# Performance work log

Measured on AMD Instinct MI355X. Metric: run time of the kernel, lower is better.

## Reference

```python
import jax, jax.numpy as jnp
import numpy as np

B, C, H, W = 32, 512, 32, 32  # in_dims = token_dim = 512, num_heads = 1
D = 512  # token_dim * num_heads
EPS = 1e-12  # torch F.normalize eps


def l2norm(x, axis):
    n = jnp.sqrt(jnp.sum(x * x, axis=axis, keepdims=True))
    return x / jnp.maximum(n, EPS)


def setup_inputs() -> dict:
    key = jax.random.key(0)
    ks = jax.random.split(key, 10)
    s = 1.0 / np.sqrt(D)
    return {
        "x_4d": jax.random.normal(ks[0], (B, C, H, W), dtype=jnp.float32),
        "Wq": jax.random.uniform(ks[1], (D, D), jnp.float32, -s, s),
        "bq": jax.random.uniform(ks[2], (D,), jnp.float32, -s, s),
        "Wk": jax.random.uniform(ks[3], (D, D), jnp.float32, -s, s),
        "bk": jax.random.uniform(ks[4], (D,), jnp.float32, -s, s),
        "w_g": jax.random.normal(ks[5], (D, 1), dtype=jnp.float32),
        "Wp": jax.random.uniform(ks[6], (D, D), jnp.float32, -s, s),
        "bp": jax.random.uniform(ks[7], (D,), jnp.float32, -s, s),
        "Wf": jax.random.uniform(ks[8], (D, D), jnp.float32, -s, s),
        "bf": jax.random.uniform(ks[9], (D,), jnp.float32, -s, s),
    }


def reference(x_4d, Wq, bq, Wk, bk, w_g, Wp, bp, Wf, bf):
    b, c, h, w = x_4d.shape
    n = h * w
    scale = D ** (-0.5)
    x = x_4d.reshape(b, c, n).transpose(0, 2, 1)  # [b, n, c]
    query = l2norm(jnp.einsum("bnc,dc->bnd", x, Wq) + bq, axis=-1)  # [b, n, d]
    key = l2norm(jnp.einsum("bnc,dc->bnd", x, Wk) + bk, axis=-1)    # [b, n, d]
    query_weight = query @ w_g                      # [b, n, 1]
    a = l2norm(query_weight * scale, axis=1)        # normalize over sequence dim
    g = jnp.sum(a * query, axis=1)                  # [b, d] global context
    out = jnp.einsum("bnd,ed->bne", g[:, None, :] * key, Wp) + bp + query
    out = jnp.einsum("bnd,ed->bne", out, Wf) + bf
    return out.transpose(0, 2, 1).reshape(b, c, h, w)
```

## Files before the change

kernel.cpp:

```cpp
#include <hip/hip_runtime.h>
#include <hip/hip_bf16.h>
#include <math.h>

#define B_ 32
#define D_ 512
#define N_ 1024
#define T_ 32768
#define SCALE 0.04419417382415922f

typedef unsigned short u16;
typedef __attribute__((ext_vector_type(8))) short bf16x8;
typedef __attribute__((ext_vector_type(4))) float f32x4;
typedef __attribute__((ext_vector_type(8))) unsigned short u16x8;
typedef __attribute__((ext_vector_type(4))) unsigned int u32x4;

__device__ __forceinline__ u16 bf16_rn(float f) {
    unsigned u = __float_as_uint(f);
    u += 0x7FFFu + ((u >> 16) & 1u);
    return (u16)(u >> 16);
}
__device__ __forceinline__ float bf16f(u16 h) {
    return __uint_as_float(((unsigned)h) << 16);
}
__device__ __forceinline__ unsigned pkbf(float a, float b) {
    __hip_bfloat162 h = __float22bfloat162_rn(make_float2(a, b));
    return *reinterpret_cast<unsigned*>(&h);
}

__device__ __forceinline__ void g2l16(const u16* g, u16* lds) {
    __builtin_amdgcn_global_load_lds(
        (const __attribute__((address_space(1))) unsigned int*)g,
        (__attribute__((address_space(3))) unsigned int*)lds, 16, 0, 0);
}

__device__ __forceinline__ float waveRedSum(float v) {
#pragma unroll
    for (int off = 32; off > 0; off >>= 1) v += __shfl_xor(v, off, 64);
    return v;
}
__device__ __forceinline__ float rnorm_s(float ssq) {
    return 1.f / fmaxf(sqrtf(ssq), 1e-12f);
}


__global__ __launch_bounds__(256) void convw_k(const float* __restrict__ W0,
                                               const float* __restrict__ W1,
                                               const float* __restrict__ W2,
                                               u16* O0, u16* O1, u16* O2) {
    const int s = blockIdx.y;
    const float* src = (s == 0) ? W0 : ((s == 1) ? W1 : W2);
    u16* O = (s == 0) ? O0 : ((s == 1) ? O1 : O2);
    const size_t i0 = (size_t)blockIdx.x * 2048 + threadIdx.x * 8;
    u16 o[8];
#pragma unroll
    for (int j = 0; j < 8; ++j) o[j] = bf16_rn(src[i0 + j]);
    *(u16x8*)&O[i0] = *(const u16x8*)&o[0];
}


__global__ __launch_bounds__(512) void gctx_k(const float* __restrict__ ssqQ,
                                              const float* __restrict__ qwr,
                                              const u16* __restrict__ Qn,
                                              float* __restrict__ g) {
    __shared__ float coeff[128];
    const int b = blockIdx.y;
    const int n0 = blockIdx.x * 128;
    const int d = threadIdx.x;
    if (d < 128) {
        const int r = b * N_ + n0 + d;
        const float rq = rnorm_s(ssqQ[r]);
        coeff[d] = qwr[r] * rq * rq;
    }
    __syncthreads();
    const u16* qp = Qn + ((size_t)b * N_ + n0) * D_ + d;
    float acc = 0.f;
    for (int n = 0; n < 128; ++n) acc += coeff[n] * bf16f(qp[(size_t)n * D_]);
    atomicAdd(g + b * D_ + d, acc);
}

__global__ __launch_bounds__(256) void scalewp_k(const float* __restrict__ Wp,
                                                 const float* __restrict__ g,
                                                 const float* __restrict__ ssqQ,
                                                 const float* __restrict__ qwr,
                                                 u16* __restrict__ WpG) {
    __shared__ float red[4];
    const int b = blockIdx.y;
    float s = 0.f;
#pragma unroll
    for (int j = 0; j < 4; ++j) {
        const int r = b * N_ + threadIdx.x * 4 + j;
        const float t = qwr[r] * rnorm_s(ssqQ[r]);
        s += t * t;
    }
    s = waveRedSum(s);
    if ((threadIdx.x & 63) == 0) red[threadIdx.x >> 6] = s;
    __syncthreads();
    const float S = red[0] + red[1] + red[2] + red[3];
    const float fb = SCALE / fmaxf(SCALE * sqrtf(S), 1e-12f);
    const size_t f0 = (size_t)blockIdx.x * 2048 + threadIdx.x * 8;
    const int c = (int)(f0 & 511);
    u16 o[8];
#pragma unroll
    for (int j = 0; j < 8; ++j)
        o[j] = bf16_rn(Wp[f0 + j] * g[b * D_ + c + j] * fb);
    *(u16x8*)&WpG[(size_t)b * 262144 + f0] = *(const u16x8*)&o[0];
}

__global__ __launch_bounds__(512, 4) void mgemm0(
        const float* __restrict__ x, const u16* __restrict__ B0,
        const u16* __restrict__ B1,
        const float* __restrict__ bias0, const float* __restrict__ bias1,
        const float* __restrict__ wg,
        float* __restrict__ ssqQ, float* __restrict__ ssqK,
        float* __restrict__ qwr, u16* uout0, u16* uout1) {
    __shared__ u16 As[128 * 64];
    __shared__ u16 Bs[256 * 64];
    const int tid = threadIdx.x;
    const int l = tid & 63, w = tid >> 6;
    const int gid = blockIdx.x;
    const int xcd = gid & 7;
    const int bx = (gid >> 3) & 3;
    const int by = (gid >> 5) * 8 + xcd;
    const int t0 = by * 128;
    const bool sel = bx >= 2;
    const int e0 = (bx & 1) * 256;
    const u16* B = sel ? B1 : B0;
    const float* bias = sel ? bias1 : bias0;
    u16* uout = sel ? uout1 : uout0;
    float* ssq = sel ? ssqK : ssqQ;
    const int batch0 = t0 >> 10;

    const float* xbase = x + (((size_t)(batch0 * D_ + w * 8)) << 10) +
                         (t0 & 1023) + 2 * l;
    const int r0 = 2 * l, r1 = 2 * l + 1;
    const int sA = w ^ (l & 7);
    u16* wA0 = &As[r0 * 64 + sA * 8];
    u16* wA1 = &As[r1 * 64 + sA * 8];
    size_t gB[4];
    u16* ldsB[4];
#pragma unroll
    for (int i = 0; i < 4; ++i) {
        const int rr = w * 32 + i * 8 + (l >> 3);
        gB[i] = (size_t)(e0 + rr) * 512 + (((l & 7) ^ (rr & 7)) * 8);
        ldsB[i] = Bs + (w * 32 + i * 8) * 64;
    }

    const int wr = w >> 2, wc = w & 3, kg = l >> 4, r16 = l & 15;
    int aoff[4][2], boff[4][2];
#pragma unroll
    for (int f = 0; f < 4; ++f)
#pragma unroll
        for (int h = 0; h < 2; ++h) {
            const int ra = wr * 64 + f * 16 + r16;
            aoff[f][h] = ra * 64 + (((h * 4 + kg) ^ ((ra >> 1) & 7)) * 8);
            const int rb = wc * 64 + f * 16 + r16;
            boff[f][h] = rb * 64 + (((h * 4 + kg) ^ (rb & 7)) * 8);
        }

    f32x4 acc[4][4];
#pragma unroll
    for (int i = 0; i < 4; ++i)
#pragma unroll
        for (int j = 0; j < 4; ++j) acc[i][j] = 0.f;

    float2 va[8];
#pragma unroll
    for (int j = 0; j < 8; ++j)
        va[j] = *(const float2*)(xbase + ((size_t)j << 10));

#pragma unroll 1
    for (int s = 0; s < 8; ++s) {
        const int c0 = s * 64;
        __syncthreads();
        {
            u32x4 p0, p1;
#pragma unroll
            for (int jj = 0; jj < 4; ++jj) {
                p0[jj] = pkbf(va[2 * jj].x, va[2 * jj + 1].x);
                p1[jj] = pkbf(va[2 * jj].y, va[2 * jj + 1].y);
            }
            *(u32x4*)wA0 = p0;
            *(u32x4*)wA1 = p1;
        }
#pragma unroll
        for (int i = 0; i < 4; ++i) g2l16(B + gB[i] + c0, ldsB[i]);
        __syncthreads();
        if (s < 7) {
#pragma unroll
            for (int j = 0; j < 8; ++j)
                va[j] = *(const float2*)(xbase + ((size_t)(c0 + 64 + j) << 10));
        }
#pragma unroll
        for (int h = 0; h < 2; ++h) {
            bf16x8 av[4], bv[4];
#pragma unroll
            for (int f = 0; f < 4; ++f) {
                av[f] = *(const bf16x8*)&As[aoff[f][h]];
                bv[f] = *(const bf16x8*)&Bs[boff[f][h]];
            }
#pragma unroll
            for (int i = 0; i < 4; ++i)
#pragma unroll
                for (int j = 0; j < 4; ++j)
                    acc[i][j] = __builtin_amdgcn_mfma_f32_16x16x32_bf16(
                        av[i], bv[j], acc[i][j], 0, 0, 0);
        }
    }

    const int mb = wr * 64 + kg * 4;
    const int nb = wc * 64 + r16;
    float bb[4], wgv[4];
#pragma unroll
    for (int fn = 0; fn < 4; ++fn) {
        const int n = e0 + nb + fn * 16;
        bb[fn] = bias[n];
        wgv[fn] = sel ? 0.f : wg[n];
    }
#pragma unroll
    for (int fm = 0; fm < 4; ++fm) {
#pragma unroll
        for (int q = 0; q < 4; ++q) {
            const int m = t0 + mb + fm * 16 + q;
            float s2 = 0.f, wd = 0.f;
#pragma unroll
            for (int fn = 0; fn < 4; ++fn) {
                const float val = acc[fm][fn][q] + bb[fn];
                uout[(size_t)m * 512 + e0 + nb + fn * 16] = bf16_rn(val);
                s2 += val * val;
                wd += val * wgv[fn];
            }
#pragma unroll
            for (int off = 1; off < 16; off <<= 1)
                s2 += __shfl_xor(s2, off, 64);
            if (!sel) {
#pragma unroll
                for (int off = 1; off < 16; off <<= 1)
                    wd += __shfl_xor(wd, off, 64);
            }
            if (r16 == 0) {
                atomicAdd(ssq + m, s2);
                if (!sel) atomicAdd(qwr + m, wd);
            }
        }
    }
}

template <int MODE>
__global__ __launch_bounds__(256) void mgemm12(
        const u16* __restrict__ A, const u16* __restrict__ B0,
        const float* __restrict__ bias,
        const float* __restrict__ rsA, const float* __restrict__ rsQ,
        u16* uout, float* __restrict__ fout) {
    __shared__ u16 As[128 * 64];
    __shared__ u16 Bs[128 * 64];
    const int tid = threadIdx.x;
    const int l = tid & 63, w = tid >> 6;
    const int gid = blockIdx.x;
    const int xcd = gid & 7;

    int rowt, col, batch;
    if (MODE == 1) {
        const int j = gid >> 3;
        batch = (j >> 5) * 8 + xcd;
        const int r = j & 31;
        rowt = batch * 8 + (r >> 2);
        col = r & 3;
    } else {
        col = (gid >> 3) & 3;
        rowt = (gid >> 5) * 8 + xcd;
        batch = rowt >> 3;
    }
    const int tt0 = rowt * 128;
    const int e0 = col * 128;
    const u16* B = (MODE == 1) ? B0 + (size_t)batch * 262144 : B0;
    const int arow0 = (MODE == 2) ? e0 : tt0;
    const int brow0 = (MODE == 2) ? tt0 : e0;

    size_t gA[4], gB[4];
    u16 *ldsA[4], *ldsB[4];
#pragma unroll
    for (int i = 0; i < 4; ++i) {
        const int rr = w * 32 + i * 8 + (l >> 3);
        const int sw = ((l & 7) ^ (rr & 7)) * 8;
        gA[i] = (size_t)(arow0 + rr) * 512 + sw;
        gB[i] = (size_t)(brow0 + rr) * 512 + sw;
        ldsA[i] = As + (w * 32 + i * 8) * 64;
        ldsB[i] = Bs + (w * 32 + i * 8) * 64;
    }

    const int wr = w >> 1, wc = w & 1, kg = l >> 4, r16 = l & 15;
    int aoff[4][2], boff[4][2];
#pragma unroll
    for (int f = 0; f < 4; ++f)
#pragma unroll
        for (int h = 0; h < 2; ++h) {
            const int ra = wr * 64 + f * 16 + r16;
            aoff[f][h] = ra * 64 + (((h * 4 + kg) ^ (ra & 7)) * 8);
            const int rb = wc * 64 + f * 16 + r16;
            boff[f][h] = rb * 64 + (((h * 4 + kg) ^ (rb & 7)) * 8);
        }

    f32x4 acc[4][4];
#pragma unroll
    for (int i = 0; i < 4; ++i)
#pragma unroll
        for (int j = 0; j < 4; ++j) acc[i][j] = 0.f;

#pragma unroll 1
    for (int c0 = 0; c0 < 512; c0 += 64) {
        __syncthreads();
#pragma unroll
        for (int i = 0; i < 4; ++i) {
            g2l16(A + gA[i] + c0, ldsA[i]);
            g2l16(B + gB[i] + c0, ldsB[i]);
        }
        __syncthreads();
#pragma unroll
        for (int h = 0; h < 2; ++h) {
            bf16x8 av[4], bv[4];
#pragma unroll
            for (int f = 0; f < 4; ++f) {
                av[f] = *(const bf16x8*)&As[aoff[f][h]];
                bv[f] = *(const bf16x8*)&Bs[boff[f][h]];
            }
#pragma unroll
            for (int i = 0; i < 4; ++i)
#pragma unroll
                for (int j = 0; j < 4; ++j)
                    acc[i][j] = __builtin_amdgcn_mfma_f32_16x16x32_bf16(
                        av[i], bv[j], acc[i][j], 0, 0, 0);
        }
    }

    const int mb = wr * 64 + kg * 4;
    const int nb = wc * 64 + r16;
    if (MODE == 1) {
#pragma unroll
        for (int fm = 0; fm < 4; ++fm) {
            const int m0 = tt0 + mb + fm * 16;
            const float4 ra4 = *(const float4*)(rsA + m0);
            const float4 rq4 = *(const float4*)(rsQ + m0);
            const float ra_[4] = {rnorm_s(ra4.x), rnorm_s(ra4.y),
                                  rnorm_s(ra4.z), rnorm_s(ra4.w)};
            const float rq_[4] = {rnorm_s(rq4.x), rnorm_s(rq4.y),
                                  rnorm_s(rq4.z), rnorm_s(rq4.w)};
#pragma unroll
            for (int fn = 0; fn < 4; ++fn) {
                const int n = e0 + nb + fn * 16;
                const float bb = bias[n];
#pragma unroll
                for (int q = 0; q < 4; ++q) {
                    const size_t idx = (size_t)(m0 + q) * 512 + n;
                    const float val = acc[fm][fn][q] * ra_[q] + bb +
                                      bf16f(uout[idx]) * rq_[q];
                    uout[idx] = bf16_rn(val);
                }
            }
        }
    } else {
#pragma unroll
        for (int fm = 0; fm < 4; ++fm)
#pragma unroll
            for (int fn = 0; fn < 4; ++fn) {
                const int ntok = (tt0 & 1023) + nb + fn * 16;
#pragma unroll
                for (int q = 0; q < 4; ++q) {
                    const int e = e0 + mb + fm * 16 + q;
                    fout[((size_t)(batch * D_ + e) << 10) + ntok] =
                        acc[fm][fn][q] + bias[e];
                }
            }
    }
}


extern "C" void kernel_launch(void* const* d_in, const int* in_sizes, int n_in,
                              void* d_out, int out_size, void* d_ws, size_t ws_size,
                              hipStream_t stream) {
    const float* x  = (const float*)d_in[0];
    const float* Wq = (const float*)d_in[1];
    const float* bq = (const float*)d_in[2];
    const float* Wk = (const float*)d_in[3];
    const float* bk = (const float*)d_in[4];
    const float* wg = (const float*)d_in[5];
    const float* Wp = (const float*)d_in[6];
    const float* bp = (const float*)d_in[7];
    const float* Wf = (const float*)d_in[8];
    const float* bf = (const float*)d_in[9];
    float* out = (float*)d_out;

    char* Wb = (char*)d_ws;
    u16* WpG = (u16*)Wb;
    u16* Qn  = (u16*)(Wb + 33554432ull);
    u16* Kn  = (u16*)(Wb + 67108864ull);
    char* S  = Wb + 100663296ull;
    u16* Wqbf = (u16*)S;
    u16* Wkbf = (u16*)(S + 524288ull);
    u16* Wfbf = (u16*)(S + 1048576ull);
    char* Z   = S + 1572864ull;
    float* SSQQ = (float*)Z;
    float* SSQK = (float*)(Z + 131072ull);
    float* QWR  = (float*)(Z + 262144ull);
    float* G    = (float*)(Z + 393216ull);
    const size_t ZBYTES = 458752ull;

    const dim3 blk(256);

    convw_k<<<dim3(128, 3), blk, 0, stream>>>(Wq, Wk, Wf, Wqbf, Wkbf, Wfbf);
    hipMemsetAsync(Z, 0, ZBYTES, stream);
    mgemm0<<<dim3(1024), dim3(512), 0, stream>>>(x, Wqbf, Wkbf, bq, bk, wg,
                                                 SSQQ, SSQK, QWR, Qn, Kn);
    gctx_k<<<dim3(8, B_), dim3(512), 0, stream>>>(SSQQ, QWR, Qn, G);
    scalewp_k<<<dim3(128, B_), blk, 0, stream>>>(Wp, G, SSQQ, QWR, WpG);
    mgemm12<1><<<dim3(1024), blk, 0, stream>>>(Kn, WpG, bp, SSQK, SSQQ, Qn,
                                               nullptr);
    mgemm12<2><<<dim3(1024), blk, 0, stream>>>(Wfbf, Qn, bf, nullptr, nullptr,
                                               nullptr, out);
}
```

Before: 154.2 us.

## Pre-transpose x to bf16 and switch GEMM staging to register prefetch

Adds a separate kernel that transposes and converts the fp32 input x into a token-major bf16 buffer, so the first GEMM loads A tiles with direct global-to-LDS copies instead of converting strided fp32 loads in-loop. The weight (B) operand in mgemm0 and both operands in mgemm12 are now loaded into registers one K-step ahead and stored to LDS, replacing the async global_load_lds path. This adds an extra pass over x (read fp32, write bf16) and a launch, and removes the occupancy hint of 4 blocks per CU from mgemm0. The aim is cheaper A staging in mgemm0 and overlapping global loads with MFMA compute.

After: 170.8 us. 1.11x slower.

```diff
diff --git a/kernel.cpp b/kernel.cpp
--- a/kernel.cpp
+++ b/kernel.cpp
@@ -1,5 +1,4 @@
 #include <hip/hip_runtime.h>
-#include <hip/hip_bf16.h>
 #include <math.h>
 
 #define B_ 32
@@ -22,10 +21,6 @@
 __device__ __forceinline__ float bf16f(u16 h) {
     return __uint_as_float(((unsigned)h) << 16);
 }
-__device__ __forceinline__ unsigned pkbf(float a, float b) {
-    __hip_bfloat162 h = __float22bfloat162_rn(make_float2(a, b));
-    return *reinterpret_cast<unsigned*>(&h);
-}
 
 __device__ __forceinline__ void g2l16(const u16* g, u16* lds) {
     __builtin_amdgcn_global_load_lds(
@@ -42,6 +37,25 @@
     return 1.f / fmaxf(sqrtf(ssq), 1e-12f);
 }
 
+
+__global__ __launch_bounds__(256) void convx_k(const float* __restrict__ x,
+                                               u16* __restrict__ X) {
+    __shared__ float tile[64][65];
+    const int tid = threadIdx.x;
+    const int n0 = blockIdx.x * 64, c0 = blockIdx.y * 64, b = blockIdx.z;
+    const int nl = tid & 63, cl0 = (tid >> 6) * 16;
+#pragma unroll
+    for (int j = 0; j < 16; ++j)
+        tile[cl0 + j][nl] = x[((size_t)(b * D_ + c0 + cl0 + j) << 10) + n0 + nl];
+    __syncthreads();
+    const int nr = tid >> 2, cb = (tid & 3) * 16;
+    const size_t row = (size_t)(b * N_ + n0 + nr) * D_ + c0 + cb;
+    u16 th[16];
+#pragma unroll
+    for (int j = 0; j < 16; ++j) th[j] = bf16_rn(tile[cb + j][nr]);
+    *(u16x8*)&X[row]     = *(const u16x8*)&th[0];
+    *(u16x8*)&X[row + 8] = *(const u16x8*)&th[8];
+}
 
 __global__ __launch_bounds__(256) void convw_k(const float* __restrict__ W0,
                                                const float* __restrict__ W1,
@@ -103,11 +117,11 @@
 #pragma unroll
     for (int j = 0; j < 8; ++j)
         o[j] = bf16_rn(Wp[f0 + j] * g[b * D_ + c + j] * fb);
-    *(u16x8*)&WpG[(size_t)b * 262144 + f0] = *(const u16x8*)&o[0];
-}
-
-__global__ __launch_bounds__(512, 4) void mgemm0(
-        const float* __restrict__ x, const u16* __restrict__ B0,
+    *(u16x8*)&WpG[(size_t)b * 262144ull + f0] = *(const u16x8*)&o[0];
+}
+
+__global__ __launch_bounds__(512) void mgemm0(
+        const u16* __restrict__ A, const u16* __restrict__ B0,
         const u16* __restrict__ B1,
         const float* __restrict__ bias0, const float* __restrict__ bias1,
         const float* __restrict__ wg,
@@ -128,21 +142,20 @@
     const float* bias = sel ? bias1 : bias0;
     u16* uout = sel ? uout1 : uout0;
     float* ssq = sel ? ssqK : ssqQ;
-    const int batch0 = t0 >> 10;
-
-    const float* xbase = x + (((size_t)(batch0 * D_ + w * 8)) << 10) +
-                         (t0 & 1023) + 2 * l;
-    const int r0 = 2 * l, r1 = 2 * l + 1;
-    const int sA = w ^ (l & 7);
-    u16* wA0 = &As[r0 * 64 + sA * 8];
-    u16* wA1 = &As[r1 * 64 + sA * 8];
-    size_t gB[4];
-    u16* ldsB[4];
+
+    size_t gA[2], gB[4];
+    u16 *ldsA[2], *wB[4];
+#pragma unroll
+    for (int i = 0; i < 2; ++i) {
+        const int rr = w * 16 + i * 8 + (l >> 3);
+        gA[i] = (size_t)(t0 + rr) * 512 + (((l & 7) ^ (rr & 7)) * 8);
+        ldsA[i] = As + (w * 16 + i * 8) * 64;
+    }
 #pragma unroll
     for (int i = 0; i < 4; ++i) {
         const int rr = w * 32 + i * 8 + (l >> 3);
         gB[i] = (size_t)(e0 + rr) * 512 + (((l & 7) ^ (rr & 7)) * 8);
-        ldsB[i] = Bs + (w * 32 + i * 8) * 64;
+        wB[i] = Bs + (w * 32 + i * 8) * 64 + l * 8;
     }
 
     const int wr = w >> 2, wc = w & 3, kg = l >> 4, r16 = l & 15;
@@ -152,7 +165,7 @@
 #pragma unroll
         for (int h = 0; h < 2; ++h) {
             const int ra = wr * 64 + f * 16 + r16;
-            aoff[f][h] = ra * 64 + (((h * 4 + kg) ^ ((ra >> 1) & 7)) * 8);
+            aoff[f][h] = ra * 64 + (((h * 4 + kg) ^ (ra & 7)) * 8);
             const int rb = wc * 64 + f * 16 + r16;
             boff[f][h] = rb * 64 + (((h * 4 + kg) ^ (rb & 7)) * 8);
         }
@@ -163,32 +176,22 @@
 #pragma unroll
         for (int j = 0; j < 4; ++j) acc[i][j] = 0.f;
 
-    float2 va[8];
-#pragma unroll
-    for (int j = 0; j < 8; ++j)
-        va[j] = *(const float2*)(xbase + ((size_t)j << 10));
+    u32x4 bpf[4];
+#pragma unroll
+    for (int i = 0; i < 4; ++i) bpf[i] = *(const u32x4*)(B + gB[i]);
 
 #pragma unroll 1
-    for (int s = 0; s < 8; ++s) {
-        const int c0 = s * 64;
+    for (int c0 = 0; c0 < 512; c0 += 64) {
         __syncthreads();
-        {
-            u32x4 p0, p1;
-#pragma unroll
-            for (int jj = 0; jj < 4; ++jj) {
-                p0[jj] = pkbf(va[2 * jj].x, va[2 * jj + 1].x);
-                p1[jj] = pkbf(va[2 * jj].y, va[2 * jj + 1].y);
-            }
-            *(u32x4*)wA0 = p0;
-            *(u32x4*)wA1 = p1;
-        }
-#pragma unroll
-        for (int i = 0; i < 4; ++i) g2l16(B + gB[i] + c0, ldsB[i]);
+#pragma unroll
+        for (int i = 0; i < 4; ++i) *(u32x4*)wB[i] = bpf[i];
+#pragma unroll
+        for (int i = 0; i < 2; ++i) g2l16(A + gA[i] + c0, ldsA[i]);
         __syncthreads();
-        if (s < 7) {
-#pragma unroll
-            for (int j = 0; j < 8; ++j)
-                va[j] = *(const float2*)(xbase + ((size_t)(c0 + 64 + j) << 10));
+        if (c0 < 448) {
+#pragma unroll
+            for (int i = 0; i < 4; ++i)
+                bpf[i] = *(const u32x4*)(B + gB[i] + c0 + 64);
         }
 #pragma unroll
         for (int h = 0; h < 2; ++h) {
@@ -272,20 +275,20 @@
     }
     const int tt0 = rowt * 128;
     const int e0 = col * 128;
-    const u16* B = (MODE == 1) ? B0 + (size_t)batch * 262144 : B0;
+    const u16* B = (MODE == 1) ? B0 + (size_t)batch * 262144ull : B0;
     const int arow0 = (MODE == 2) ? e0 : tt0;
     const int brow0 = (MODE == 2) ? tt0 : e0;
 
     size_t gA[4], gB[4];
-    u16 *ldsA[4], *ldsB[4];
+    u16 *wA[4], *wBp[4];
 #pragma unroll
     for (int i = 0; i < 4; ++i) {
         const int rr = w * 32 + i * 8 + (l >> 3);
         const int sw = ((l & 7) ^ (rr & 7)) * 8;
         gA[i] = (size_t)(arow0 + rr) * 512 + sw;
         gB[i] = (size_t)(brow0 + rr) * 512 + sw;
-        ldsA[i] = As + (w * 32 + i * 8) * 64;
-        ldsB[i] = Bs + (w * 32 + i * 8) * 64;
+        wA[i]  = As + (w * 32 + i * 8) * 64 + l * 8;
+        wBp[i] = Bs + (w * 32 + i * 8) * 64 + l * 8;
     }
 
     const int wr = w >> 1, wc = w & 1, kg = l >> 4, r16 = l & 15;
@@ -306,15 +309,29 @@
 #pragma unroll
         for (int j = 0; j < 4; ++j) acc[i][j] = 0.f;
 
+    u32x4 apf[4], bpf[4];
+#pragma unroll
+    for (int i = 0; i < 4; ++i) {
+        apf[i] = *(const u32x4*)(A + gA[i]);
+        bpf[i] = *(const u32x4*)(B + gB[i]);
+    }
+
 #pragma unroll 1
     for (int c0 = 0; c0 < 512; c0 += 64) {
         __syncthreads();
 #pragma unroll
         for (int i = 0; i < 4; ++i) {
-            g2l16(A + gA[i] + c0, ldsA[i]);
-            g2l16(B + gB[i] + c0, ldsB[i]);
+            *(u32x4*)wA[i]  = apf[i];
+            *(u32x4*)wBp[i] = bpf[i];
         }
         __syncthreads();
+        if (c0 < 448) {
+#pragma unroll
+            for (int i = 0; i < 4; ++i) {
+                apf[i] = *(const u32x4*)(A + gA[i] + c0 + 64);
+                bpf[i] = *(const u32x4*)(B + gB[i] + c0 + 64);
+            }
+        }
 #pragma unroll
         for (int h = 0; h < 2; ++h) {
             bf16x8 av[4], bv[4];
@@ -390,6 +407,7 @@
     float* out = (float*)d_out;
 
     char* Wb = (char*)d_ws;
+    u16* Xbf = (u16*)Wb;
     u16* WpG = (u16*)Wb;
     u16* Qn  = (u16*)(Wb + 33554432ull);
     u16* Kn  = (u16*)(Wb + 67108864ull);
@@ -406,9 +424,10 @@
 
     const dim3 blk(256);
 
+    convx_k<<<dim3(16, 8, 32), blk, 0, stream>>>(x, Xbf);
     convw_k<<<dim3(128, 3), blk, 0, stream>>>(Wq, Wk, Wf, Wqbf, Wkbf, Wfbf);
     hipMemsetAsync(Z, 0, ZBYTES, stream);
-    mgemm0<<<dim3(1024), dim3(512), 0, stream>>>(x, Wqbf, Wkbf, bq, bk, wg,
+    mgemm0<<<dim3(1024), dim3(512), 0, stream>>>(Xbf, Wqbf, Wkbf, bq, bk, wg,
                                                  SSQQ, SSQK, QWR, Qn, Kn);
     gctx_k<<<dim3(8, B_), dim3(512), 0, stream>>>(SSQQ, QWR, Qn, G);
     scalewp_k<<<dim3(128, B_), blk, 0, stream>>>(Wp, G, SSQQ, QWR, WpG);
```
